# Kernel tuning notes

Measured on AMD Instinct MI355X. Metric: run time of the kernel, lower is better.

Reference implementation:

```python
import jax, jax.numpy as jnp
import numpy as np

# ---- static structure (from operand_label_matrices shapes; labels = unique ints) ----
SHAPES = [(256, 256), (256, 256), (256, 256)]
SIZES = [h * w for h, w in SHAPES]
OFFS = np.cumsum([0] + SIZES)          # global flat offset of each matrix
N_ELEM = int(OFFS[-1])                  # 196608
LANE = 8                                # memory_lane_width
N_ROWS = -(-N_ELEM // LANE)             # ceil -> 24576 (divisible by 4)
H_T, W_T = SHAPES[-1]
NUM_OPS = H_T * W_T                     # 65536
BATCH = 8

_ii, _jj = np.meshgrid(np.arange(H_T), np.arange(W_T), indexing='ij')
DST_IDX = (OFFS[len(SHAPES) - 1] + (_ii * W_T + _jj)).ravel()
SRC_IDX = np.stack([OFFS[m] + (_ii % SHAPES[m][0]) * SHAPES[m][1] + (_jj % SHAPES[m][1])
                    for m in range(len(SHAPES) - 1)], axis=-1).reshape(NUM_OPS, -1)
SEQ_IDX = np.concatenate([SRC_IDX, DST_IDX[:, None]], axis=1)  # [NUM_OPS, n_src+1]


def _conv2d(x, w, b):
    y = jax.lax.conv_general_dilated(x, w, (1, 1), 'SAME',
                                     dimension_numbers=('NCHW', 'OIHW', 'NCHW'))
    return y + b[None, :, None, None]


def _pl_logprob(logits, order):
    # Plackett-Luce log-prob of a full permutation: closed form of the
    # sequential log_softmax + (-inf)-masking loop in the torch code.
    s = logits[order]
    return jnp.sum(s - jax.lax.cumlogsumexp(s, reverse=True))


def _tier_mult(h):
    # cache_line=2, l1=4, l2=8, l3=16
    return jnp.where(h <= 2, 1.0, jnp.where(h <= 4, 1.5,
           jnp.where(h <= 8, 2.0, jnp.where(h <= 16, 3.0, 5.0))))


def _staged(fwd, bwd, fwd_exp, bwd_exp):
    return jnp.sum(fwd ** fwd_exp * _tier_mult(fwd)) + jnp.sum(bwd ** bwd_exp * _tier_mult(bwd))


def _single(mem_logits, g_mem, g_op, pm_w, pm_b, mc_w, mc_b, pj_w, pj_b):
    # --- memory-address permutation (Gumbel-perturbed argsort) ---
    perm = jnp.argsort(mem_logits + g_mem)          # addr of element i = perm[i]
    mem_lp = _pl_logprob(mem_logits, perm)
    # --- per-matrix conv features + per-element scatter into memory space ---
    mem_flat = jnp.zeros((8, N_ROWS * LANE), jnp.float32)
    for m, (H, W) in enumerate(SHAPES):
        addrs = perm[OFFS[m]:OFFS[m + 1]]
        inp = addrs.astype(jnp.float32).reshape(1, 1, H, W)
        feat = jax.nn.relu(_conv2d(inp, pm_w[m], pm_b[m]))   # [1,8,H,W]
        mem_flat = mem_flat.at[:, addrs].set(feat.reshape(8, H * W))
    mem_space = mem_flat.reshape(1, 8, N_ROWS, LANE)
    # --- conv / adaptive-avg-pool(4,4) / proj ---
    mc = jax.nn.relu(_conv2d(mem_space, mc_w, mc_b))         # [1,16,N_ROWS,LANE]
    pooled = mc.reshape(16, 4, N_ROWS // 4, 4, LANE // 4).mean(axis=(2, 4))  # [16,4,4]
    op_logits = pj_w @ pooled.reshape(-1) + pj_b             # [NUM_OPS]
    # --- op permutation ---
    op_order = jnp.argsort(op_logits + g_op)
    op_lp = _pl_logprob(op_logits, op_order)
    # --- hop penalties over ordered ops ---
    seq = perm[SEQ_IDX][op_order].astype(jnp.float32)        # [NUM_OPS, L]
    inter = seq[1:, 0] - seq[:-1, -1]                        # next op first src - prev dst
    intra = (seq[:, 1:] - seq[:, :-1]).reshape(-1)
    inter_pen = _staged(jax.nn.relu(inter), jax.nn.relu(-inter), 1.0, 2.0)
    intra_pen = _staged(jax.nn.relu(intra), jax.nn.relu(-intra), 1.0, 2.0)
    return inter_pen, intra_pen, op_lp, mem_lp


def setup_inputs() -> dict:
    key = jax.random.key(0)
    ks = jax.random.split(key, 9)
    return {
        'mem_logits': jax.random.normal(ks[0], (BATCH, N_ELEM), jnp.float32),
        'gumbel_mem': jax.random.gumbel(ks[1], (BATCH, N_ELEM), jnp.float32),
        'gumbel_op': jax.random.gumbel(ks[2], (BATCH, NUM_OPS), jnp.float32),
        'pm_conv_w': jax.random.normal(ks[3], (3, 8, 1, 3, 3), jnp.float32) * 0.2,
        'pm_conv_b': jax.random.normal(ks[4], (3, 8), jnp.float32) * 0.05,
        'mem_conv_w': jax.random.normal(ks[5], (16, 8, 3, 3), jnp.float32) * 0.1,
        'mem_conv_b': jax.random.normal(ks[6], (16,), jnp.float32) * 0.05,
        'proj_w': jax.random.normal(ks[7], (NUM_OPS, 256), jnp.float32) * 0.02,
        'proj_b': jax.random.normal(ks[8], (NUM_OPS,), jnp.float32) * 0.02,
    }


def reference(mem_logits, gumbel_mem, gumbel_op, pm_conv_w, pm_conv_b,
              mem_conv_w, mem_conv_b, proj_w, proj_b):
    fn = jax.vmap(_single, in_axes=(0, 0, 0, None, None, None, None, None, None))
    inter_pen, intra_pen, op_lp, mem_lp = fn(mem_logits, gumbel_mem, gumbel_op,
                                             pm_conv_w, pm_conv_b, mem_conv_w,
                                             mem_conv_b, proj_w, proj_b)
    # rows: inter_pen, intra_pen, op_logprobs, mem_logprobs, each [BATCH]
    return jnp.stack([inter_pen, intra_pen, op_lp, mem_lp])
```

## Files before the change

### kernel.cpp

```cpp
#include <hip/hip_runtime.h>
#include <math.h>

#define NB 8
#define NMEM 196608
#define NOP 65536
#define NBLK_MEM 768
#define LSEG 512
#define EPB 4096
#define NC_MEM 48
#define NC_OP 16

static __device__ __forceinline__ unsigned keymap(float f) {
  unsigned u = __float_as_uint(f);
  return (u & 0x80000000u) ? ~u : (u | 0x80000000u);
}

static __device__ __forceinline__ void comb(float& M1, float& T1, float M2, float T2) {
  if (T2 == 0.f) return;
  if (T1 == 0.f) { M1 = M2; T1 = T2; return; }
  float M = fmaxf(M1, M2);
  T1 = T1 * expf(M1 - M) + T2 * expf(M2 - M);
  M1 = M;
}

__global__ void k_zero(double* acc) {
  if (threadIdx.x < 32) acc[threadIdx.x] = 0.0;
}

__global__ void k_radix_hist0(const float* __restrict__ ml, const float* __restrict__ gm,
                              unsigned* __restrict__ hist) {
  __shared__ unsigned h[256];
  int batch = blockIdx.x % NB, cb = blockIdx.x / NB;
  int t = threadIdx.x;
  h[t] = 0;
  __syncthreads();
  const float* pm = ml + (size_t)batch * NMEM + (size_t)cb * EPB;
  const float* pg = gm + (size_t)batch * NMEM + (size_t)cb * EPB;
  #pragma unroll
  for (int r = 0; r < 16; r++) {
    unsigned key = keymap(pm[r * 256 + t] + pg[r * 256 + t]);
    atomicAdd(&h[key & 255u], 1u);
  }
  __syncthreads();
  hist[((size_t)batch * 256 + t) * NC_MEM + cb] = h[t];
}

__global__ void k_radix_hist(const unsigned long long* __restrict__ src, unsigned* __restrict__ hist,
                             int nper, int nblk, int shift) {
  __shared__ unsigned h[256];
  int batch = blockIdx.x % NB, cb = blockIdx.x / NB;
  int t = threadIdx.x;
  h[t] = 0;
  __syncthreads();
  const unsigned long long* p = src + (size_t)batch * nper + (size_t)cb * EPB;
  #pragma unroll
  for (int r = 0; r < 16; r++) {
    unsigned long long v = p[r * 256 + t];
    unsigned d = (unsigned)(v >> shift) & 255u;
    atomicAdd(&h[d], 1u);
  }
  __syncthreads();
  hist[((size_t)batch * 256 + t) * nblk + cb] = h[t];
}

__global__ void __launch_bounds__(1024) k_radix_scan(unsigned* __restrict__ hist, int L) {
  int b = blockIdx.x, t = threadIdx.x;
  unsigned* h = hist + (size_t)b * L;
  int C = L / 1024;
  unsigned s = 0;
  for (int i = 0; i < C; i++) s += h[t * C + i];
  __shared__ unsigned ls[1024];
  ls[t] = s;
  __syncthreads();
  for (int off = 1; off < 1024; off <<= 1) {
    unsigned add = (t >= off) ? ls[t - off] : 0u;
    __syncthreads();
    ls[t] += add;
    __syncthreads();
  }
  unsigned run = (t > 0) ? ls[t - 1] : 0u;
  for (int i = 0; i < C; i++) { unsigned v = h[t * C + i]; h[t * C + i] = run; run += v; }
}

#define SCATTER_BODY(GETV, WRITE)                                              \
  __shared__ unsigned base[256];                                               \
  __shared__ unsigned run[256];                                                \
  __shared__ unsigned wh[4][256];                                              \
  int t = threadIdx.x, lane = t & 63, wv = t >> 6;                             \
  base[t] = hist[((size_t)batch * 256 + t) * nblk + cb];                       \
  run[t] = 0;                                                                  \
  unsigned long long v[16];                                                    \
  GETV;                                                                        \
  __syncthreads();                                                             \
  _Pragma("unroll")                                                            \
  for (int r = 0; r < 16; r++) {                                               \
    unsigned d = (unsigned)(v[r] >> shift) & 255u;                             \
    unsigned long long m = ~0ull;                                              \
    _Pragma("unroll")                                                          \
    for (int bit = 0; bit < 8; bit++) {                                        \
      unsigned long long bal = __ballot((d >> bit) & 1u);                      \
      m &= ((d >> bit) & 1u) ? bal : ~bal;                                     \
    }                                                                          \
    unsigned rank = (unsigned)__popcll(m & ((1ull << lane) - 1ull));           \
    _Pragma("unroll")                                                          \
    for (int w = 0; w < 4; w++) wh[w][t] = 0;                                  \
    __syncthreads();                                                           \
    if (rank == 0) wh[wv][d] = (unsigned)__popcll(m);                          \
    __syncthreads();                                                           \
    {                                                                          \
      unsigned run_t = run[t];                                                 \
      _Pragma("unroll")                                                        \
      for (int w = 0; w < 4; w++) { unsigned x = wh[w][t]; wh[w][t] = run_t; run_t += x; } \
      run[t] = run_t;                                                          \
    }                                                                          \
    __syncthreads();                                                           \
    unsigned pos = base[d] + wh[wv][d] + rank;                                 \
    WRITE;                                                                     \
    __syncthreads();                                                           \
  }

__global__ void k_radix_scatter0(const float* __restrict__ ml, const float* __restrict__ gm,
                                 unsigned long long* __restrict__ dst, const unsigned* __restrict__ hist) {
  int batch = blockIdx.x % NB, cb = blockIdx.x / NB;
  const int nblk = NC_MEM, shift = 32;
  const float* pm = ml + (size_t)batch * NMEM + (size_t)cb * EPB;
  const float* pg = gm + (size_t)batch * NMEM + (size_t)cb * EPB;
  unsigned long long* q = dst + (size_t)batch * NMEM;
  SCATTER_BODY(
    { _Pragma("unroll")
      for (int r = 0; r < 16; r++) {
        unsigned key = keymap(pm[r * 256 + t] + pg[r * 256 + t]);
        v[r] = ((unsigned long long)key << 32) | (unsigned)(cb * EPB + r * 256 + t);
      } },
    { q[pos] = v[r]; })
}

__global__ void k_radix_scatter(const unsigned long long* __restrict__ src, unsigned long long* __restrict__ dst,
                                const unsigned* __restrict__ hist, int nper, int nblk, int shift) {
  int batch = blockIdx.x % NB, cb = blockIdx.x / NB;
  const unsigned long long* p = src + (size_t)batch * nper + (size_t)cb * EPB;
  unsigned long long* q = dst + (size_t)batch * nper;
  SCATTER_BODY(
    { _Pragma("unroll")
      for (int r = 0; r < 16; r++) v[r] = p[r * 256 + t]; },
    { q[pos] = v[r]; })
}

__global__ void k_radix_scatter_lo(const unsigned long long* __restrict__ src, unsigned* __restrict__ dst,
                                   const unsigned* __restrict__ hist, int nper, int nblk) {
  int batch = blockIdx.x % NB, cb = blockIdx.x / NB;
  const int shift = 56;
  const unsigned long long* p = src + (size_t)batch * nper + (size_t)cb * EPB;
  unsigned* q = dst + (size_t)batch * nper;
  SCATTER_BODY(
    { _Pragma("unroll")
      for (int r = 0; r < 16; r++) v[r] = p[r * 256 + t]; },
    { q[pos] = (unsigned)v[r]; })
}

__global__ void kpl_seg(const float* __restrict__ logits, const unsigned* __restrict__ order,
                        int n, int nseg, float* __restrict__ segM, float* __restrict__ segT,
                        float* __restrict__ slog, double* __restrict__ acc, int row) {
  int b = blockIdx.x % NB;
  int sg = blockIdx.x / NB;
  int t = threadIdx.x, lane = t & 63, wv = t >> 6;
  int seg = sg * 4 + wv;
  const float* lg = logits + (size_t)b * n;
  const unsigned* od = order + (size_t)b * n + (size_t)seg * LSEG + lane * 8;
  uint4 i0 = *((const uint4*)od);
  uint4 i1 = *((const uint4*)(od + 4));
  float s0 = lg[i0.x], s1 = lg[i0.y], s2 = lg[i0.z], s3 = lg[i0.w];
  float s4 = lg[i1.x], s5 = lg[i1.y], s6 = lg[i1.z], s7 = lg[i1.w];
  float* sl = slog + (size_t)b * n + (size_t)seg * LSEG + lane * 8;
  *((float4*)sl) = make_float4(s0, s1, s2, s3);
  *((float4*)(sl + 4)) = make_float4(s4, s5, s6, s7);
  float m = fmaxf(fmaxf(fmaxf(s0, s1), fmaxf(s2, s3)),
                  fmaxf(fmaxf(s4, s5), fmaxf(s6, s7)));
  float T = expf(s0 - m) + expf(s1 - m) + expf(s2 - m) + expf(s3 - m)
          + expf(s4 - m) + expf(s5 - m) + expf(s6 - m) + expf(s7 - m);
  double ss = ((double)s0 + (double)s1) + ((double)s2 + (double)s3)
            + ((double)s4 + (double)s5) + ((double)s6 + (double)s7);
  #pragma unroll
  for (int off = 1; off < 64; off <<= 1) {
    float M2 = __shfl_xor(m, off);
    float T2 = __shfl_xor(T, off);
    comb(m, T, M2, T2);
    ss += __shfl_xor(ss, off);
  }
  __shared__ double sw[4];
  if (lane == 0) { segM[b * nseg + seg] = m; segT[b * nseg + seg] = T; sw[wv] = ss; }
  __syncthreads();
  if (t == 0) atomicAdd(&acc[row * 8 + b], (sw[0] + sw[1]) + (sw[2] + sw[3]));
}

__global__ void __launch_bounds__(512) kpl_scan(const float* __restrict__ segM, const float* __restrict__ segT,
                                                int nseg, float* __restrict__ sufM, float* __restrict__ sufT) {
  int b = blockIdx.x, t = threadIdx.x;
  __shared__ float sm[512], st_[512];
  float M = -INFINITY, T = 0.f;
  if (t < nseg) { M = segM[b * nseg + t]; T = segT[b * nseg + t]; }
  sm[t] = M; st_[t] = T;
  __syncthreads();
  for (int off = 1; off < 512; off <<= 1) {
    float M2 = -INFINITY, T2 = 0.f;
    if (t + off < 512) { M2 = sm[t + off]; T2 = st_[t + off]; }
    __syncthreads();
    comb(M, T, M2, T2);
    sm[t] = M; st_[t] = T;
    __syncthreads();
  }
  if (t < nseg) {
    float eM = -INFINITY, eT = 0.f;
    if (t + 1 < nseg) { eM = sm[t + 1]; eT = st_[t + 1]; }
    sufM[b * nseg + t] = eM; sufT[b * nseg + t] = eT;
  }
}

__global__ void kpl_main(const float* __restrict__ slog, int n, int nseg,
                         const float* __restrict__ sufM, const float* __restrict__ sufT,
                         double* __restrict__ acc, int row) {
  int b = blockIdx.x % NB;
  int sg = blockIdx.x / NB;
  int t = threadIdx.x, lane = t & 63, wv = t >> 6;
  int seg = sg * 4 + wv;
  const float* sl = slog + (size_t)b * n + (size_t)seg * LSEG + lane * 8;
  float4 a = *((const float4*)sl);
  float4 c = *((const float4*)(sl + 4));
  float s[8] = {a.x, a.y, a.z, a.w, c.x, c.y, c.z, c.w};
  float m = fmaxf(fmaxf(fmaxf(s[0], s[1]), fmaxf(s[2], s[3])),
                  fmaxf(fmaxf(s[4], s[5]), fmaxf(s[6], s[7])));
  float T = expf(s[0] - m) + expf(s[1] - m) + expf(s[2] - m) + expf(s[3] - m)
          + expf(s[4] - m) + expf(s[5] - m) + expf(s[6] - m) + expf(s[7] - m);
  #pragma unroll
  for (int off = 1; off < 64; off <<= 1) {
    float M2 = __shfl_down(m, off);
    float T2 = __shfl_down(T, off);
    if (lane + off < 64) comb(m, T, M2, T2);
  }
  float Mx = __shfl_down(m, 1);
  float Tx = __shfl_down(T, 1);
  if (lane == 63) { Mx = -INFINITY; Tx = 0.f; }
  comb(Mx, Tx, sufM[b * nseg + seg], sufT[b * nseg + seg]);
  float Ms[8], Ts[8];
  #pragma unroll
  for (int i = 7; i >= 0; i--) {
    float sv = s[i];
    if (Tx == 0.f) { Mx = sv; Tx = 1.f; }
    else if (sv > Mx) { Tx = Tx * expf(Mx - sv) + 1.f; Mx = sv; }
    else Tx += expf(sv - Mx);
    Ms[i] = Mx; Ts[i] = Tx;
  }
  double lsum = 0.0;
  #pragma unroll
  for (int i = 0; i < 8; i++) lsum += (double)Ms[i] + (double)logf(Ts[i]);
  #pragma unroll
  for (int off = 1; off < 64; off <<= 1) lsum += __shfl_xor(lsum, off);
  __shared__ double sw[4];
  if (lane == 0) sw[wv] = lsum;
  __syncthreads();
  if (t == 0) atomicAdd(&acc[row * 8 + b], -((sw[0] + sw[1]) + (sw[2] + sw[3])));
}

__global__ void k_conv1b(const unsigned* __restrict__ permg, const float* __restrict__ pmw,
                         const float* __restrict__ pmb, float* __restrict__ mf) {
  int t = threadIdx.x;
  int b4 = blockIdx.x / NBLK_MEM;
  int g0 = (blockIdx.x % NBLK_MEM) * 256;
  int mm = g0 >> 16;
  int p = (g0 & 65535) + t;
  int i = p >> 8, j = p & 255;
  const unsigned* ad = permg + (size_t)b4 * NMEM + mm * 65536;
  float nb[3][3];
  #pragma unroll
  for (int di = 0; di < 3; di++)
    #pragma unroll
    for (int dj = 0; dj < 3; dj++) {
      int ii = i + di - 1, jj = j + dj - 1;
      nb[di][dj] = (ii >= 0 && ii < 256 && jj >= 0 && jj < 256) ? (float)ad[ii * 256 + jj] : 0.f;
    }
  unsigned c = ad[p];
  float o[8];
  #pragma unroll
  for (int oc = 0; oc < 8; oc++) {
    float s = pmb[mm * 8 + oc];
    #pragma unroll
    for (int di = 0; di < 3; di++)
      #pragma unroll
      for (int dj = 0; dj < 3; dj++)
        s += pmw[mm * 72 + oc * 9 + di * 3 + dj] * nb[di][dj];
    o[oc] = fmaxf(s, 0.f);
  }
  float4* dst = (float4*)(mf + ((size_t)b4 * NMEM + c) * 8);
  dst[0] = make_float4(o[0], o[1], o[2], o[3]);
  dst[1] = make_float4(o[4], o[5], o[6], o[7]);
}

__global__ void k_conv2b(const float* __restrict__ mf, const float* __restrict__ mcw,
                         const float* __restrict__ mcb, double* __restrict__ part, int gb) {
  __shared__ float pw[4][16][4];
  int t = threadIdx.x;
  int b4 = blockIdx.x / NBLK_MEM;
  int blk = blockIdx.x % NBLK_MEM;
  int r = blk * 32 + (t >> 3);
  int l = t & 7;
  const float* base = mf + (size_t)b4 * (NMEM * 8);
  float nb[9][8];
  #pragma unroll
  for (int q = 0; q < 9; q++) {
    int rr = r + q / 3 - 1, ll = l + q % 3 - 1;
    if (rr >= 0 && rr < 24576 && ll >= 0 && ll < 8) {
      const float4* px = (const float4*)(base + ((size_t)rr * 8 + ll) * 8);
      float4 a = px[0], bb = px[1];
      nb[q][0] = a.x; nb[q][1] = a.y; nb[q][2] = a.z; nb[q][3] = a.w;
      nb[q][4] = bb.x; nb[q][5] = bb.y; nb[q][6] = bb.z; nb[q][7] = bb.w;
    } else {
      #pragma unroll
      for (int c = 0; c < 8; c++) nb[q][c] = 0.f;
    }
  }
  int lane = t & 63, wv = t >> 6;
  #pragma unroll
  for (int c2 = 0; c2 < 16; c2++) {
    float s = mcb[c2];
    #pragma unroll
    for (int c = 0; c < 8; c++)
      #pragma unroll
      for (int q = 0; q < 9; q++)
        s += mcw[c2 * 72 + c * 9 + q] * nb[q][c];
    float v = fmaxf(s, 0.f);
    v += __shfl_xor(v, 1);
    v += __shfl_xor(v, 8);
    v += __shfl_xor(v, 16);
    v += __shfl_xor(v, 32);
    if ((lane & 1) == 0 && ((t >> 3) & 7) == 0) pw[wv][c2][(lane & 7) >> 1] = v;
  }
  __syncthreads();
  if (t < 64) {
    int c2 = t >> 2, d = t & 3;
    double s = (double)pw[0][c2][d] + (double)pw[1][c2][d] + (double)pw[2][c2][d] + (double)pw[3][c2][d];
    part[((size_t)(gb + b4) * NBLK_MEM + blk) * 64 + t] = s;
  }
}

__global__ void k_pool_final(const double* __restrict__ part, double* __restrict__ pooled) {
  int b = blockIdx.x, t = threadIdx.x;
  int c2 = t >> 4, a = (t >> 2) & 3, d = t & 3;
  double s = 0.0;
  for (int j = 0; j < 192; j++)
    s += part[((size_t)b * NBLK_MEM + a * 192 + j) * 64 + c2 * 4 + d];
  pooled[b * 256 + t] = s / 12288.0;
}

__global__ void k_oplogits(const float* __restrict__ pjw, const float* __restrict__ pjb,
                           const double* __restrict__ pooled, const float* __restrict__ gop,
                           float* __restrict__ oplog, unsigned long long* __restrict__ opkv) {
  __shared__ double pl[8][256];
  int t = threadIdx.x;
  #pragma unroll
  for (int b = 0; b < 8; b++) pl[b][t] = pooled[b * 256 + t];
  __syncthreads();
  int k = blockIdx.x * 256 + t;
  const float4* row = (const float4*)(pjw + (size_t)k * 256);
  double acc[8];
  #pragma unroll
  for (int b = 0; b < 8; b++) acc[b] = 0.0;
  for (int j4 = 0; j4 < 64; j4++) {
    float4 w = row[j4];
    int j = j4 * 4;
    #pragma unroll
    for (int b = 0; b < 8; b++)
      acc[b] += (double)w.x * pl[b][j] + (double)w.y * pl[b][j + 1]
              + (double)w.z * pl[b][j + 2] + (double)w.w * pl[b][j + 3];
  }
  float bias = pjb[k];
  #pragma unroll
  for (int b = 0; b < 8; b++) {
    float ol = (float)(acc[b] + (double)bias);
    oplog[(size_t)b * NOP + k] = ol;
    float key = ol + gop[(size_t)b * NOP + k];
    opkv[(size_t)b * NOP + k] = ((unsigned long long)keymap(key) << 32) | (unsigned)k;
  }
}

static __device__ __forceinline__ float tierf(float h) {
  return h <= 2.f ? 1.f : (h <= 4.f ? 1.5f : (h <= 8.f ? 2.f : (h <= 16.f ? 3.f : 5.f)));
}
static __device__ __forceinline__ double penf(float d) {
  float fwd = d > 0.f ? d : 0.f;
  float bwd = d < 0.f ? -d : 0.f;
  return (double)(fwd * tierf(fwd)) + (double)(bwd * bwd * tierf(bwd));
}

__global__ void k_pen(const unsigned* __restrict__ perm, const unsigned* __restrict__ oo,
                      double* __restrict__ acc) {
  int b = blockIdx.x % NB;
  int k = (blockIdx.x / NB) * 256 + threadIdx.x;
  const unsigned* P = perm + (size_t)b * NMEM;
  float A = (float)P[k], Bv = (float)P[NOP + k], Cv = (float)P[2 * NOP + k];
  double pi = penf(Bv - A) + penf(Cv - Bv);
  double pe = 0.0;
  if (k < 65535) {
    unsigned k0 = oo[(size_t)b * NOP + k], k1 = oo[(size_t)b * NOP + k + 1];
    pe = penf((float)P[k1] - (float)P[2 * NOP + k0]);
  }
  __shared__ double ri[256], re[256];
  ri[threadIdx.x] = pi; re[threadIdx.x] = pe;
  __syncthreads();
  for (int off = 128; off > 0; off >>= 1) {
    if (threadIdx.x < off) { ri[threadIdx.x] += ri[threadIdx.x + off]; re[threadIdx.x] += re[threadIdx.x + off]; }
    __syncthreads();
  }
  if (threadIdx.x == 0) { atomicAdd(&acc[8 + b], ri[0]); atomicAdd(&acc[0 + b], re[0]); }
}

__global__ void k_finalize(const double* __restrict__ acc, float* __restrict__ out) {
  if (threadIdx.x < 32) out[threadIdx.x] = (float)acc[threadIdx.x];
}

extern "C" void kernel_launch(void* const* d_in, const int* in_sizes, int n_in,
                              void* d_out, int out_size, void* d_ws, size_t ws_size,
                              hipStream_t stream) {
  (void)in_sizes; (void)n_in; (void)out_size; (void)ws_size;
  const float* ml  = (const float*)d_in[0];
  const float* gm  = (const float*)d_in[1];
  const float* gop = (const float*)d_in[2];
  const float* pmw = (const float*)d_in[3];
  const float* pmb = (const float*)d_in[4];
  const float* mcw = (const float*)d_in[5];
  const float* mcb = (const float*)d_in[6];
  const float* pjw = (const float*)d_in[7];
  const float* pjb = (const float*)d_in[8];
  float* out = (float*)d_out;
  char* ws = (char*)d_ws;

  unsigned long long* kvA = (unsigned long long*)(ws + 0);
  unsigned long long* kvB = (unsigned long long*)(ws + 12582912);
  unsigned* hist   = (unsigned*)(ws + 25165824);
  unsigned* perm   = (unsigned*)(ws + 31457280);
  double*   part   = (double*)(ws + 37748736);
  double*   pooled = (double*)(ws + 40894464);
  double*   acc    = (double*)(ws + 40910848);
  float*    segM   = (float*)(ws + 40911104);
  float*    segT   = (float*)(ws + 40923392);
  float*    sufM   = (float*)(ws + 40935680);
  float*    sufT   = (float*)(ws + 40947968);
  float*    slog  = (float*)(ws + 12582912);
  float* mf = (float*)(ws + 0);
  unsigned long long* opkvA = (unsigned long long*)(ws + 0);
  unsigned long long* opkvB = (unsigned long long*)(ws + 4194304);
  float*    oplog = (float*)(ws + 8388608);
  unsigned* oo    = (unsigned*)(ws + 10485760);

  k_zero<<<1, 32, 0, stream>>>(acc);

  k_radix_hist0<<<NB * NC_MEM, 256, 0, stream>>>(ml, gm, hist);
  k_radix_scan<<<NB, 1024, 0, stream>>>(hist, 256 * NC_MEM);
  k_radix_scatter0<<<NB * NC_MEM, 256, 0, stream>>>(ml, gm, kvA, hist);
  k_radix_hist<<<NB * NC_MEM, 256, 0, stream>>>(kvA, hist, NMEM, NC_MEM, 40);
  k_radix_scan<<<NB, 1024, 0, stream>>>(hist, 256 * NC_MEM);
  k_radix_scatter<<<NB * NC_MEM, 256, 0, stream>>>(kvA, kvB, hist, NMEM, NC_MEM, 40);
  k_radix_hist<<<NB * NC_MEM, 256, 0, stream>>>(kvB, hist, NMEM, NC_MEM, 48);
  k_radix_scan<<<NB, 1024, 0, stream>>>(hist, 256 * NC_MEM);
  k_radix_scatter<<<NB * NC_MEM, 256, 0, stream>>>(kvB, kvA, hist, NMEM, NC_MEM, 48);
  k_radix_hist<<<NB * NC_MEM, 256, 0, stream>>>(kvA, hist, NMEM, NC_MEM, 56);
  k_radix_scan<<<NB, 1024, 0, stream>>>(hist, 256 * NC_MEM);
  k_radix_scatter_lo<<<NB * NC_MEM, 256, 0, stream>>>(kvA, perm, hist, NMEM, NC_MEM);

  {
    int nseg = NMEM / LSEG;
    kpl_seg <<<NB * (nseg / 4), 256, 0, stream>>>(ml, perm, NMEM, nseg, segM, segT, slog, acc, 3);
    kpl_scan<<<NB, 512, 0, stream>>>(segM, segT, nseg, sufM, sufT);
    kpl_main<<<NB * (nseg / 4), 256, 0, stream>>>(slog, NMEM, nseg, sufM, sufT, acc, 3);
  }

  for (int g = 0; g < 2; g++) {
    k_conv1b<<<4 * NBLK_MEM, 256, 0, stream>>>(perm + (size_t)g * 4 * NMEM, pmw, pmb, mf);
    k_conv2b<<<4 * NBLK_MEM, 256, 0, stream>>>(mf, mcw, mcb, part, g * 4);
  }
  k_pool_final<<<NB, 256, 0, stream>>>(part, pooled);

  k_oplogits<<<NOP / 256, 256, 0, stream>>>(pjw, pjb, pooled, gop, oplog, opkvA);

  k_radix_hist<<<NB * NC_OP, 256, 0, stream>>>(opkvA, hist, NOP, NC_OP, 32);
  k_radix_scan<<<NB, 1024, 0, stream>>>(hist, 256 * NC_OP);
  k_radix_scatter<<<NB * NC_OP, 256, 0, stream>>>(opkvA, opkvB, hist, NOP, NC_OP, 32);
  k_radix_hist<<<NB * NC_OP, 256, 0, stream>>>(opkvB, hist, NOP, NC_OP, 40);
  k_radix_scan<<<NB, 1024, 0, stream>>>(hist, 256 * NC_OP);
  k_radix_scatter<<<NB * NC_OP, 256, 0, stream>>>(opkvB, opkvA, hist, NOP, NC_OP, 40);
  k_radix_hist<<<NB * NC_OP, 256, 0, stream>>>(opkvA, hist, NOP, NC_OP, 48);
  k_radix_scan<<<NB, 1024, 0, stream>>>(hist, 256 * NC_OP);
  k_radix_scatter<<<NB * NC_OP, 256, 0, stream>>>(opkvA, opkvB, hist, NOP, NC_OP, 48);
  k_radix_hist<<<NB * NC_OP, 256, 0, stream>>>(opkvB, hist, NOP, NC_OP, 56);
  k_radix_scan<<<NB, 1024, 0, stream>>>(hist, 256 * NC_OP);
  k_radix_scatter_lo<<<NB * NC_OP, 256, 0, stream>>>(opkvB, oo, hist, NOP, NC_OP);

  {
    int nseg = NOP / LSEG;
    kpl_seg <<<NB * (nseg / 4), 256, 0, stream>>>(oplog, oo, NOP, nseg, segM, segT, slog, acc, 2);
    kpl_scan<<<NB, 512, 0, stream>>>(segM, segT, nseg, sufM, sufT);
    kpl_main<<<NB * (nseg / 4), 256, 0, stream>>>(slog, NOP, nseg, sufM, sufT, acc, 2);
  }

  k_pen<<<NB * NOP / 256, 256, 0, stream>>>(perm, oo, acc);

  k_finalize<<<1, 32, 0, stream>>>(acc, out);
}
```

Measured before the change: 425.4 us.

## Fuse next-pass radix histogram into scatter and run convs in one pass

Each radix scatter pass now also accumulates the next digit's per-block histogram through global atomics, with the scan kernel zeroing the alternate histogram buffer. This removes the separate histogram kernels and their re-read of the key array. When the workspace is large enough, the two conv kernels run once over all 8 batches instead of two groups of 4, using a larger feature buffer. The cost is many contended global atomics per element in the scatter and a much larger workspace requirement.

```diff
diff --git a/kernel.cpp b/kernel.cpp
--- a/kernel.cpp
+++ b/kernel.cpp
@@ -63,10 +63,15 @@
   hist[((size_t)batch * 256 + t) * nblk + cb] = h[t];
 }
 
-__global__ void __launch_bounds__(1024) k_radix_scan(unsigned* __restrict__ hist, int L) {
+__global__ void __launch_bounds__(1024) k_radix_scan(unsigned* __restrict__ hist, int L,
+                                                     unsigned* __restrict__ zb) {
   int b = blockIdx.x, t = threadIdx.x;
   unsigned* h = hist + (size_t)b * L;
   int C = L / 1024;
+  if (zb) {
+    unsigned* z = zb + (size_t)b * L;
+    for (int i = 0; i < C; i++) z[t * C + i] = 0u;
+  }
   unsigned s = 0;
   for (int i = 0; i < C; i++) s += h[t * C + i];
   __shared__ unsigned ls[1024];
@@ -119,8 +124,9 @@
     __syncthreads();                                                           \
   }
 
-__global__ void k_radix_scatter0(const float* __restrict__ ml, const float* __restrict__ gm,
-                                 unsigned long long* __restrict__ dst, const unsigned* __restrict__ hist) {
+__global__ void k_radix_scatter0h(const float* __restrict__ ml, const float* __restrict__ gm,
+                                  unsigned long long* __restrict__ dst, const unsigned* __restrict__ hist,
+                                  unsigned* __restrict__ hist2, int nshift) {
   int batch = blockIdx.x % NB, cb = blockIdx.x / NB;
   const int nblk = NC_MEM, shift = 32;
   const float* pm = ml + (size_t)batch * NMEM + (size_t)cb * EPB;
@@ -132,18 +138,21 @@
         unsigned key = keymap(pm[r * 256 + t] + pg[r * 256 + t]);
         v[r] = ((unsigned long long)key << 32) | (unsigned)(cb * EPB + r * 256 + t);
       } },
-    { q[pos] = v[r]; })
-}
-
-__global__ void k_radix_scatter(const unsigned long long* __restrict__ src, unsigned long long* __restrict__ dst,
-                                const unsigned* __restrict__ hist, int nper, int nblk, int shift) {
+    { q[pos] = v[r];
+      atomicAdd(&hist2[((size_t)batch * 256 + ((unsigned)(v[r] >> nshift) & 255u)) * nblk + (pos >> 12)], 1u); })
+}
+
+__global__ void k_radix_scatterh(const unsigned long long* __restrict__ src, unsigned long long* __restrict__ dst,
+                                 const unsigned* __restrict__ hist, int nper, int nblk, int shift,
+                                 unsigned* __restrict__ hist2, int nshift) {
   int batch = blockIdx.x % NB, cb = blockIdx.x / NB;
   const unsigned long long* p = src + (size_t)batch * nper + (size_t)cb * EPB;
   unsigned long long* q = dst + (size_t)batch * nper;
   SCATTER_BODY(
     { _Pragma("unroll")
       for (int r = 0; r < 16; r++) v[r] = p[r * 256 + t]; },
-    { q[pos] = v[r]; })
+    { q[pos] = v[r];
+      atomicAdd(&hist2[((size_t)batch * 256 + ((unsigned)(v[r] >> nshift) & 255u)) * nblk + (pos >> 12)], 1u); })
 }
 
 __global__ void k_radix_scatter_lo(const unsigned long long* __restrict__ src, unsigned* __restrict__ dst,
@@ -420,7 +429,7 @@
 extern "C" void kernel_launch(void* const* d_in, const int* in_sizes, int n_in,
                               void* d_out, int out_size, void* d_ws, size_t ws_size,
                               hipStream_t stream) {
-  (void)in_sizes; (void)n_in; (void)out_size; (void)ws_size;
+  (void)in_sizes; (void)n_in; (void)out_size;
   const float* ml  = (const float*)d_in[0];
   const float* gm  = (const float*)d_in[1];
   const float* gop = (const float*)d_in[2];
@@ -435,7 +444,8 @@
 
   unsigned long long* kvA = (unsigned long long*)(ws + 0);
   unsigned long long* kvB = (unsigned long long*)(ws + 12582912);
-  unsigned* hist   = (unsigned*)(ws + 25165824);
+  unsigned* histA  = (unsigned*)(ws + 25165824);
+  unsigned* histB  = (unsigned*)(ws + 25559040);
   unsigned* perm   = (unsigned*)(ws + 31457280);
   double*   part   = (double*)(ws + 37748736);
   double*   pooled = (double*)(ws + 40894464);
@@ -445,26 +455,28 @@
   float*    sufM   = (float*)(ws + 40935680);
   float*    sufT   = (float*)(ws + 40947968);
   float*    slog  = (float*)(ws + 12582912);
-  float* mf = (float*)(ws + 0);
+  float* mfsmall = (float*)(ws + 0);
+  float* mfbig   = (float*)(ws + 67108864);
   unsigned long long* opkvA = (unsigned long long*)(ws + 0);
   unsigned long long* opkvB = (unsigned long long*)(ws + 4194304);
   float*    oplog = (float*)(ws + 8388608);
   unsigned* oo    = (unsigned*)(ws + 10485760);
+  const size_t need_big = 67108864ull + (size_t)NB * NMEM * 8 * 4;
 
   k_zero<<<1, 32, 0, stream>>>(acc);
 
-  k_radix_hist0<<<NB * NC_MEM, 256, 0, stream>>>(ml, gm, hist);
-  k_radix_scan<<<NB, 1024, 0, stream>>>(hist, 256 * NC_MEM);
-  k_radix_scatter0<<<NB * NC_MEM, 256, 0, stream>>>(ml, gm, kvA, hist);
-  k_radix_hist<<<NB * NC_MEM, 256, 0, stream>>>(kvA, hist, NMEM, NC_MEM, 40);
-  k_radix_scan<<<NB, 1024, 0, stream>>>(hist, 256 * NC_MEM);
-  k_radix_scatter<<<NB * NC_MEM, 256, 0, stream>>>(kvA, kvB, hist, NMEM, NC_MEM, 40);
-  k_radix_hist<<<NB * NC_MEM, 256, 0, stream>>>(kvB, hist, NMEM, NC_MEM, 48);
-  k_radix_scan<<<NB, 1024, 0, stream>>>(hist, 256 * NC_MEM);
-  k_radix_scatter<<<NB * NC_MEM, 256, 0, stream>>>(kvB, kvA, hist, NMEM, NC_MEM, 48);
-  k_radix_hist<<<NB * NC_MEM, 256, 0, stream>>>(kvA, hist, NMEM, NC_MEM, 56);
-  k_radix_scan<<<NB, 1024, 0, stream>>>(hist, 256 * NC_MEM);
-  k_radix_scatter_lo<<<NB * NC_MEM, 256, 0, stream>>>(kvA, perm, hist, NMEM, NC_MEM);
+  {
+    const int L = 256 * NC_MEM;
+    k_radix_hist0<<<NB * NC_MEM, 256, 0, stream>>>(ml, gm, histA);
+    k_radix_scan<<<NB, 1024, 0, stream>>>(histA, L, histB);
+    k_radix_scatter0h<<<NB * NC_MEM, 256, 0, stream>>>(ml, gm, kvA, histA, histB, 40);
+    k_radix_scan<<<NB, 1024, 0, stream>>>(histB, L, histA);
+    k_radix_scatterh<<<NB * NC_MEM, 256, 0, stream>>>(kvA, kvB, histB, NMEM, NC_MEM, 40, histA, 48);
+    k_radix_scan<<<NB, 1024, 0, stream>>>(histA, L, histB);
+    k_radix_scatterh<<<NB * NC_MEM, 256, 0, stream>>>(kvB, kvA, histA, NMEM, NC_MEM, 48, histB, 56);
+    k_radix_scan<<<NB, 1024, 0, stream>>>(histB, L, (unsigned*)0);
+    k_radix_scatter_lo<<<NB * NC_MEM, 256, 0, stream>>>(kvA, perm, histB, NMEM, NC_MEM);
+  }
 
   {
     int nseg = NMEM / LSEG;
@@ -473,26 +485,31 @@
     kpl_main<<<NB * (nseg / 4), 256, 0, stream>>>(slog, NMEM, nseg, sufM, sufT, acc, 3);
   }
 
-  for (int g = 0; g < 2; g++) {
-    k_conv1b<<<4 * NBLK_MEM, 256, 0, stream>>>(perm + (size_t)g * 4 * NMEM, pmw, pmb, mf);
-    k_conv2b<<<4 * NBLK_MEM, 256, 0, stream>>>(mf, mcw, mcb, part, g * 4);
+  if (ws_size >= need_big) {
+    k_conv1b<<<NB * NBLK_MEM, 256, 0, stream>>>(perm, pmw, pmb, mfbig);
+    k_conv2b<<<NB * NBLK_MEM, 256, 0, stream>>>(mfbig, mcw, mcb, part, 0);
+  } else {
+    for (int g = 0; g < 2; g++) {
+      k_conv1b<<<4 * NBLK_MEM, 256, 0, stream>>>(perm + (size_t)g * 4 * NMEM, pmw, pmb, mfsmall);
+      k_conv2b<<<4 * NBLK_MEM, 256, 0, stream>>>(mfsmall, mcw, mcb, part, g * 4);
+    }
   }
   k_pool_final<<<NB, 256, 0, stream>>>(part, pooled);
 
   k_oplogits<<<NOP / 256, 256, 0, stream>>>(pjw, pjb, pooled, gop, oplog, opkvA);
 
-  k_radix_hist<<<NB * NC_OP, 256, 0, stream>>>(opkvA, hist, NOP, NC_OP, 32);
-  k_radix_scan<<<NB, 1024, 0, stream>>>(hist, 256 * NC_OP);
-  k_radix_scatter<<<NB * NC_OP, 256, 0, stream>>>(opkvA, opkvB, hist, NOP, NC_OP, 32);
-  k_radix_hist<<<NB * NC_OP, 256, 0, stream>>>(opkvB, hist, NOP, NC_OP, 40);
-  k_radix_scan<<<NB, 1024, 0, stream>>>(hist, 256 * NC_OP);
-  k_radix_scatter<<<NB * NC_OP, 256, 0, stream>>>(opkvB, opkvA, hist, NOP, NC_OP, 40);
-  k_radix_hist<<<NB * NC_OP, 256, 0, stream>>>(opkvA, hist, NOP, NC_OP, 48);
-  k_radix_scan<<<NB, 1024, 0, stream>>>(hist, 256 * NC_OP);
-  k_radix_scatter<<<NB * NC_OP, 256, 0, stream>>>(opkvA, opkvB, hist, NOP, NC_OP, 48);
-  k_radix_hist<<<NB * NC_OP, 256, 0, stream>>>(opkvB, hist, NOP, NC_OP, 56);
-  k_radix_scan<<<NB, 1024, 0, stream>>>(hist, 256 * NC_OP);
-  k_radix_scatter_lo<<<NB * NC_OP, 256, 0, stream>>>(opkvB, oo, hist, NOP, NC_OP);
+  {
+    const int L = 256 * NC_OP;
+    k_radix_hist<<<NB * NC_OP, 256, 0, stream>>>(opkvA, histA, NOP, NC_OP, 32);
+    k_radix_scan<<<NB, 1024, 0, stream>>>(histA, L, histB);
+    k_radix_scatterh<<<NB * NC_OP, 256, 0, stream>>>(opkvA, opkvB, histA, NOP, NC_OP, 32, histB, 40);
+    k_radix_scan<<<NB, 1024, 0, stream>>>(histB, L, histA);
+    k_radix_scatterh<<<NB * NC_OP, 256, 0, stream>>>(opkvB, opkvA, histB, NOP, NC_OP, 40, histA, 48);
+    k_radix_scan<<<NB, 1024, 0, stream>>>(histA, L, histB);
+    k_radix_scatterh<<<NB * NC_OP, 256, 0, stream>>>(opkvA, opkvB, histA, NOP, NC_OP, 48, histB, 56);
+    k_radix_scan<<<NB, 1024, 0, stream>>>(histB, L, (unsigned*)0);
+    k_radix_scatter_lo<<<NB * NC_OP, 256, 0, stream>>>(opkvB, oo, histB, NOP, NC_OP);
+  }
 
   {
     int nseg = NOP / LSEG;
```

Result: slower. 688.1 us (+61.8%).
